# Kernel tuning notes

Hardware: AMD Instinct MI355X
Metric: run time of the kernel (lower is better)

Reference implementation:

```python
import jax, jax.numpy as jnp
from jax import lax
import numpy as np

IOU_TH = 0.5
SCORE_TH = 0.05
MAX_PER_CLASS = 10
MAX_TOTAL = 10
K_PRE = 200  # pre-NMS candidates per class (>> max_output_size_per_class)


def make_anchors(image_size: int) -> jnp.ndarray:
    """Replicates AnchorBoxes.create_anchors_boxes for square images (static shapes)."""
    aspect_ratios = [0.5, 1.0, 2.0]
    scales = [2.0 ** 0, 2.0 ** (1.0 / 3.0), 2.0 ** (2.0 / 3.0)]
    step = (image_size - 32) // 4
    areas = [(x * step + 32) ** 2 for x in range(5)]
    strides = [2 ** i for i in range(3, 8)]
    levels = []
    for l in range(5):
        fs = int(np.ceil(image_size / strides[l]))
        dims = []
        for r in aspect_ratios:  # order matches TF code: ratio outer, scale inner
            h = np.sqrt(areas[l] / r)
            w = areas[l] / h
            for s in scales:
                dims.append([s * w, s * h])
        dims = np.asarray(dims, np.float32)  # [9, 2]
        c = (np.arange(fs, dtype=np.float32) + 0.5) * strides[l]
        X, Y = np.meshgrid(c, c)  # 'xy' indexing, as in tf.meshgrid default
        centers = np.stack([X, Y], -1)  # [fs, fs, 2] (cx, cy)
        centers = np.broadcast_to(centers[:, :, None, :], (fs, fs, 9, 2))
        d = np.broadcast_to(dims[None, None], (fs, fs, 9, 2))
        levels.append(np.concatenate([centers, d], -1).reshape(-1, 4))
    return jnp.asarray(np.concatenate(levels, 0))  # [N, 4] (cx, cy, w, h)


def pairwise_iou(b):  # b: [..., K, 4] in corner format
    lt = jnp.maximum(b[..., :, None, :2], b[..., None, :, :2])
    rb = jnp.minimum(b[..., :, None, 2:], b[..., None, :, 2:])
    wh = jnp.clip(rb - lt, 0.0)
    inter = wh[..., 0] * wh[..., 1]
    area = (b[..., 2] - b[..., 0]) * (b[..., 3] - b[..., 1])
    union = area[..., :, None] + area[..., None, :] - inter
    return inter / jnp.maximum(union, 1e-8)


def setup_inputs() -> dict:
    key = jax.random.key(0)
    k1, k2 = jax.random.split(key)
    images = jax.random.normal(k1, (32, 512, 512, 3), dtype=jnp.float32)
    predictions = jax.random.normal(k2, (32, 49104, 7), dtype=jnp.float32)
    return {"images": images, "predictions": predictions}


def reference(images, predictions):
    B = predictions.shape[0]
    anchors = make_anchors(images.shape[1])  # [N, 4], static shape
    box_var = jnp.asarray([0.1, 0.1, 0.2, 0.2], predictions.dtype)

    # Decode boxes.
    bp = predictions[:, :, :4] * box_var
    cls = jax.nn.sigmoid(predictions[:, :, 4:])  # [B, N, C]
    a = anchors[None]
    xy = bp[..., :2] * a[..., 2:] + a[..., :2]
    wh = jnp.exp(bp[..., 2:]) * a[..., 2:]
    boxes = jnp.concatenate([xy - wh / 2.0, xy + wh / 2.0], -1)  # [B, N, 4] corners

    # Combined NMS (class-aware, shared boxes q=1).
    scores = jnp.transpose(cls, (0, 2, 1))  # [B, C, N]
    C = scores.shape[1]
    top_s, top_i = lax.top_k(scores, K_PRE)  # [B, C, K]
    bK = jnp.take_along_axis(boxes[:, None], top_i[..., None], axis=2)  # [B, C, K, 4]
    iou = pairwise_iou(bK)  # [B, C, K, K]
    valid = top_s >= SCORE_TH
    idx = jnp.arange(K_PRE)

    def body(i, keep):
        alive = keep[..., i][..., None]
        suppress = (iou[..., i, :] > IOU_TH) & alive & (idx > i)
        return keep & ~suppress

    keep = lax.fori_loop(0, K_PRE, body, valid)
    sel = jnp.where(keep, top_s, -1.0)

    pc_s, pc_i = lax.top_k(sel, MAX_PER_CLASS)  # [B, C, 10]
    pc_b = jnp.take_along_axis(bK, pc_i[..., None], axis=2)  # [B, C, 10, 4]
    pc_c = jnp.broadcast_to(jnp.arange(C, dtype=jnp.float32)[None, :, None], pc_s.shape)

    flat_s = pc_s.reshape(B, -1)
    flat_b = pc_b.reshape(B, -1, 4)
    flat_c = pc_c.reshape(B, -1)
    fs, fi = lax.top_k(flat_s, MAX_TOTAL)  # [B, 10]
    fb = jnp.take_along_axis(flat_b, fi[..., None], axis=1)
    fc = jnp.take_along_axis(flat_c, fi, axis=1)

    valid_mask = fs > 0.0
    nmsed_boxes = jnp.where(valid_mask[..., None], fb, 0.0)
    nmsed_scores = jnp.where(valid_mask, fs, 0.0)
    nmsed_classes = jnp.where(valid_mask, fc, 0.0)
    valid_detections = jnp.sum(valid_mask, axis=-1).astype(jnp.int32)
    return nmsed_boxes, nmsed_scores, nmsed_classes, valid_detections
```

## Files before the change

### kernel.cpp

```cpp
#include <hip/hip_runtime.h>
#include <math.h>

#define NA      49104
#define NB      32
#define KPRE    200
#define CAP     2048
#define NSLICE  64
#define NQ4     85932
#define PERQ    1344
#define STHR    448
#define TAU     2.0f
#define NBINS   512
#define SLOTCAP 64

#define WS_CNT   0
#define WS_KEYS  24576
#define WS_S10   (WS_KEYS + 96*NSLICE*SLOTCAP*8)
#define WS_B10   (WS_S10 + 96*10*4)
#define WS_DONE  (WS_B10 + 96*10*16)

__device__ __forceinline__ void anchor_of(int idx, float& cx, float& cy,
                                          float& aw, float& ah) {
    int l, r;
    if (idx < 36864)      { l = 0; r = idx; }
    else if (idx < 46080) { l = 1; r = idx - 36864; }
    else if (idx < 48384) { l = 2; r = idx - 46080; }
    else if (idx < 48960) { l = 3; r = idx - 48384; }
    else                  { l = 4; r = idx - 48960; }
    const int   fss[5]     = {64, 32, 16, 8, 4};
    const int   strides[5] = {8, 16, 32, 64, 128};
    const double areas[5]  = {1024.0, 23104.0, 73984.0, 153664.0, 262144.0};
    int a    = r % 9;
    int cell = r / 9;
    int fs   = fss[l];
    int jx   = cell % fs;
    int iy   = cell / fs;
    cx = ((float)jx + 0.5f) * (float)strides[l];
    cy = ((float)iy + 0.5f) * (float)strides[l];
    int ri = a / 3, si = a % 3;
    double ratio = (ri == 0) ? 0.5 : ((ri == 1) ? 1.0 : 2.0);
    double h = sqrt(areas[l] / ratio);
    double w = areas[l] / h;
    double s = (si == 0) ? 1.0
             : ((si == 1) ? 1.2599210498948732
                          : 1.5874010519681994);
    aw = (float)(s * w);
    ah = (float)(s * h);
}

__device__ __forceinline__ int bin_of(float x) {
    int bin = (int)floorf((x + 8.0f) * 32.0f);
    return min(max(bin, 0), NBINS - 1);
}

__device__ __forceinline__ unsigned omap(float x) {
    unsigned u = __float_as_uint(x);
    return u ^ ((u >> 31) ? 0xFFFFFFFFu : 0x80000000u);
}

__device__ __forceinline__ unsigned long long shfl_xor_u64(unsigned long long v,
                                                           int m) {
    unsigned lo = (unsigned)v, hi = (unsigned)(v >> 32);
    lo = __shfl_xor(lo, m, 64);
    hi = __shfl_xor(hi, m, 64);
    return ((unsigned long long)hi << 32) | lo;
}

__global__ __launch_bounds__(STHR) void scan_kernel(
        const float* __restrict__ pred, unsigned* __restrict__ cnts,
        unsigned long long* __restrict__ keys, unsigned* __restrict__ done) {
    const int blk = blockIdx.x;
    const int b   = blk >> 6;
    const int sl  = blk & 63;
    const int tid = threadIdx.x;

    __shared__ unsigned long long stage[3][SLOTCAP];
    __shared__ unsigned scnt[3];
    if (tid < 3) scnt[tid] = 0u;
    __syncthreads();

    const int p = tid % 7;
    int cls[4];
    #pragma unroll
    for (int j = 0; j < 4; ++j) {
        int f = (4 * p + j) % 7;
        cls[j] = (f >= 4) ? (f - 4) : -1;
    }

    const float4* row = (const float4*)(pred + (size_t)b * NA * 7);
    const int q0 = sl * PERQ + tid;
    const int q1 = q0 + STHR, q2 = q1 + STHR;
    float4 v0, v1, v2;
    bool g0 = q0 < NQ4, g1 = q1 < NQ4, g2 = q2 < NQ4;
    if (g0) v0 = row[q0];
    if (g1) v1 = row[q1];
    if (g2) v2 = row[q2];

    #pragma unroll
    for (int it = 0; it < 3; ++it) {
        bool   g = (it == 0) ? g0 : (it == 1) ? g1 : g2;
        float4 v = (it == 0) ? v0 : (it == 1) ? v1 : v2;
        int    q = (it == 0) ? q0 : (it == 1) ? q1 : q2;
        if (!g) continue;
        float vv[4] = {v.x, v.y, v.z, v.w};
        #pragma unroll
        for (int j = 0; j < 4; ++j) {
            if (cls[j] >= 0 && vv[j] >= TAU) {
                int e = (q << 2) + j;
                int n = e / 7;
                unsigned u = __float_as_uint(vv[j]) | 0x80000000u;
                unsigned long long key =
                    ((unsigned long long)(~u) << 32) | (unsigned)n;
                int c = cls[j];
                unsigned pos = atomicAdd(&scnt[c], 1u);
                if (pos < SLOTCAP) stage[c][pos] = key;
            }
        }
    }
    __syncthreads();

    if (tid < 3) cnts[(b * 3 + tid) * NSLICE + sl] = scnt[tid];
    if (tid == 3 && sl == 0) done[b] = 0u;

    #pragma unroll
    for (int c = 0; c < 3; ++c) {
        unsigned n = min(scnt[c], (unsigned)SLOTCAP);
        unsigned long long* dst =
            keys + ((size_t)(b * 3 + c) * NSLICE + sl) * SLOTCAP;
        for (unsigned i = tid; i < n; i += STHR) dst[i] = stage[c][i];
    }
}

__device__ __forceinline__ void bitonic_sort(unsigned long long* buf, unsigned P,
                                             int tid) {
    for (unsigned k = 2; k <= P; k <<= 1) {
        for (unsigned j = k >> 1; j > 0; j >>= 1) {
            for (unsigned i = tid; i < P; i += 256) {
                unsigned ixj = i ^ j;
                if (ixj > i) {
                    bool up = ((i & k) == 0);
                    unsigned long long a = buf[i], bb = buf[ixj];
                    if ((a > bb) == up) { buf[i] = bb; buf[ixj] = a; }
                }
            }
            __syncthreads();
        }
    }
}

__global__ __launch_bounds__(256) void nms_merge_kernel(
        const float* __restrict__ pred, const unsigned* __restrict__ cnts,
        const unsigned long long* __restrict__ gkeys,
        float* __restrict__ s10, float4* __restrict__ b10,
        unsigned* __restrict__ done, float* __restrict__ out) {
    const int blk = blockIdx.x;
    const int tid = threadIdx.x;

    if (blk >= 96) {
        const int b = blk - 96;
        if (tid == 0) {
            while (__hip_atomic_load(&done[b], __ATOMIC_ACQUIRE,
                                     __HIP_MEMORY_SCOPE_AGENT) < 3u)
                __builtin_amdgcn_s_sleep(8);
        }
        __syncthreads();
        __threadfence();

        if (tid < 64) {
            float s = (tid < 30) ? s10[b * 30 + tid] : -2.0f;
            float* ob = out + b * 40;
            float* os = out + 1280 + b * 10;
            float* oc = out + 1600 + b * 10;
            float* ov = out + 1920 + b;
            int valid = 0;
            for (int k = 0; k < 10; ++k) {
                unsigned u = __float_as_uint(s);
                unsigned o = (u >> 31) ? ~u : (u | 0x80000000u);
                unsigned long long key =
                    ((unsigned long long)o << 6) | (unsigned)(63 - tid);
                #pragma unroll
                for (int off = 1; off < 64; off <<= 1) {
                    unsigned long long k2 = __shfl_xor(key, off, 64);
                    key = (k2 > key) ? k2 : key;
                }
                int t = 63 - (int)(key & 63ULL);
                float best = __shfl(s, t, 64);
                bool v = best > 0.0f;
                if (tid == t) {
                    float4 bb = v ? b10[b * 30 + t] : make_float4(0, 0, 0, 0);
                    ob[k * 4 + 0] = bb.x; ob[k * 4 + 1] = bb.y;
                    ob[k * 4 + 2] = bb.z; ob[k * 4 + 3] = bb.w;
                    os[k] = v ? best : 0.0f;
                    oc[k] = v ? (float)(t / 10) : 0.0f;
                    s = -2.0f;
                }
                valid += v ? 1 : 0;
            }
            if (tid == 0) ov[0] = (float)valid;
        }
        return;
    }

    const int b = blk / 3;
    const int c = blk % 3;

    __shared__ unsigned long long keybuf[CAP];
    __shared__ unsigned long long sortbuf[512];
    __shared__ float4 boxes[KPRE];
    __shared__ float  scores_s[256];
    __shared__ unsigned long long mask[256][4];
    __shared__ unsigned hist[256];
    __shared__ unsigned hist512[NBINS];
    __shared__ unsigned Lb[NSLICE], Bb[NSLICE];
    __shared__ unsigned sMn[4], sMx[4];
    __shared__ unsigned sel_thr, sel_cnt, s_prefB, s_cumB, s_M, s_sh, s_common;
    __shared__ int sT;

    for (int i = tid; i < CAP; i += 256) keybuf[i] = ~0ULL;
    for (int i = tid; i < 512; i += 256) sortbuf[i] = ~0ULL;
    for (int i = tid; i < 256; i += 256) hist[i] = 0u;
    if (tid == 0) sel_cnt = 0u;
    __syncthreads();

    if (tid < 64) {
        unsigned L  = cnts[blk * NSLICE + tid];
        unsigned Lc = min(L, (unsigned)SLOTCAP);
        unsigned pre = Lc;
        #pragma unroll
        for (int off = 1; off < 64; off <<= 1) {
            unsigned v = __shfl_up(pre, off, 64);
            if (tid >= off) pre += v;
        }
        Lb[tid] = Lc;
        Bb[tid] = pre - Lc;
        unsigned long long ob = __ballot(L > SLOTCAP);
        if (tid == 63) s_M = pre;
        if (tid == 0)  s_common = (ob == 0ULL) ? 1u : 0u;
    }
    __syncthreads();

    const unsigned M0 = s_M;
    const bool common = s_common && M0 >= KPRE && M0 <= CAP;

    if (common) {
        const unsigned long long* src = gkeys + (size_t)blk * NSLICE * SLOTCAP;
        for (int i = tid; i < NSLICE * SLOTCAP; i += 256) {
            int sl = i >> 6, k = i & (SLOTCAP - 1);
            if ((unsigned)k < Lb[sl]) keybuf[Bb[sl] + k] = src[i];
        }
    } else {
        for (int i = tid; i < NBINS; i += 256) hist512[i] = 0u;
        if (tid == 0) s_M = 0u;
        __syncthreads();
        const float* base = pred + (size_t)b * NA * 7 + 4 + c;
        for (int n = tid; n < NA; n += 256)
            atomicAdd(&hist512[bin_of(base[(size_t)n * 7])], 1u);
        __syncthreads();
        if (tid < 64) {
            unsigned h[8]; unsigned lsum = 0;
            #pragma unroll
            for (int k = 0; k < 8; ++k) { h[k] = hist512[tid*8+k]; lsum += h[k]; }
            unsigned suf = lsum;
            #pragma unroll
            for (int off = 1; off < 64; off <<= 1) {
                unsigned v = __shfl_down(suf, off, 64);
                if (tid < 64 - off) suf += v;
            }
            unsigned acc = suf - lsum;
            #pragma unroll
            for (int k = 7; k >= 0; --k) {
                unsigned na = acc + h[k];
                if (na >= KPRE && acc < KPRE) sT = max(tid*8 + k - 1, 0);
                acc = na;
            }
        }
        __syncthreads();
        const int T = sT;
        for (int n = tid; n < NA; n += 256) {
            float x = base[(size_t)n * 7];
            if (bin_of(x) >= T) {
                unsigned long long key =
                    ((unsigned long long)(~omap(x)) << 32) | (unsigned)n;
                unsigned pos = atomicAdd(&s_M, 1u);
                if (pos < CAP) keybuf[pos] = key;
            }
        }
    }
    __syncthreads();
    const unsigned M = min(s_M, (unsigned)CAP);

    if (M > KPRE) {
        {
            unsigned mn = 0xFFu, mx = 0u;
            for (int i = tid; i < (int)M; i += 256) {
                unsigned h = (unsigned)(keybuf[i] >> 56);
                mn = min(mn, h); mx = max(mx, h);
            }
            #pragma unroll
            for (int off = 1; off < 64; off <<= 1) {
                mn = min(mn, (unsigned)__shfl_xor((int)mn, off, 64));
                mx = max(mx, (unsigned)__shfl_xor((int)mx, off, 64));
            }
            if ((tid & 63) == 0) { sMn[tid >> 6] = mn; sMx[tid >> 6] = mx; }
        }
        __syncthreads();
        if (tid == 0) {
            unsigned mn = min(min(sMn[0], sMn[1]), min(sMn[2], sMn[3]));
            unsigned mx = max(max(sMx[0], sMx[1]), max(sMx[2], sMx[3]));
            s_sh = (mn == mx) ? 40u : 48u;
        }
        __syncthreads();
        const unsigned sh = s_sh;

        for (int i = tid; i < (int)M; i += 256)
            atomicAdd(&hist[(unsigned)(keybuf[i] >> (sh + 8)) & 0xFFu], 1u);
        __syncthreads();
        if (tid < 64) {
            unsigned h0 = hist[tid*4],   h1 = hist[tid*4+1];
            unsigned h2 = hist[tid*4+2], h3 = hist[tid*4+3];
            unsigned lsum = h0 + h1 + h2 + h3;
            unsigned pre = lsum;
            #pragma unroll
            for (int off = 1; off < 64; off <<= 1) {
                unsigned v = __shfl_up(pre, off, 64);
                if (tid >= off) pre += v;
            }
            unsigned acc = pre - lsum;
            if (acc < KPRE) {
                if      (acc + h0            >= KPRE) { s_prefB = tid*4;   s_cumB = acc; }
                else if (acc + h0 + h1       >= KPRE) { s_prefB = tid*4+1; s_cumB = acc+h0; }
                else if (acc + h0 + h1 + h2  >= KPRE) { s_prefB = tid*4+2; s_cumB = acc+h0+h1; }
                else if (acc + lsum          >= KPRE) { s_prefB = tid*4+3; s_cumB = acc+h0+h1+h2; }
            }
        }
        __syncthreads();
        const unsigned B = s_prefB, before = s_cumB;
        for (int i = tid; i < 256; i += 256) hist[i] = 0u;
        __syncthreads();
        for (int i = tid; i < (int)M; i += 256) {
            unsigned long long key = keybuf[i];
            if (((unsigned)(key >> (sh + 8)) & 0xFFu) == B)
                atomicAdd(&hist[(unsigned)(key >> sh) & 0xFFu], 1u);
        }
        __syncthreads();
        if (tid < 64) {
            const unsigned target = KPRE - before;
            unsigned h0 = hist[tid*4],   h1 = hist[tid*4+1];
            unsigned h2 = hist[tid*4+2], h3 = hist[tid*4+3];
            unsigned lsum = h0 + h1 + h2 + h3;
            unsigned pre = lsum;
            #pragma unroll
            for (int off = 1; off < 64; off <<= 1) {
                unsigned v = __shfl_up(pre, off, 64);
                if (tid >= off) pre += v;
            }
            unsigned acc = pre - lsum;
            if (acc < target) {
                unsigned b2 = 256;
                if      (acc + h0           >= target) b2 = tid*4;
                else if (acc + h0 + h1      >= target) b2 = tid*4+1;
                else if (acc + h0 + h1 + h2 >= target) b2 = tid*4+2;
                else if (acc + lsum         >= target) b2 = tid*4+3;
                if (b2 < 256) sel_thr = (B << 8) | b2;
            }
        }
        __syncthreads();
        const unsigned thr = sel_thr;
        for (int i = tid; i < (int)M; i += 256) {
            unsigned long long key = keybuf[i];
            if (((unsigned)(key >> sh) & 0xFFFFu) <= thr) {
                unsigned pos = atomicAdd(&sel_cnt, 1u);
                if (pos < 512) sortbuf[pos] = key;
            }
        }
        __syncthreads();
    } else {
        for (int i = tid; i < (int)M; i += 256) sortbuf[i] = keybuf[i];
        if (tid == 0) sel_cnt = M;
        __syncthreads();
    }

    const unsigned C2 = sel_cnt;
    unsigned long long* sorted;
    if (C2 <= 256) {
        unsigned long long v = (tid < (int)C2) ? sortbuf[tid] : ~0ULL;
        __syncthreads();
        #pragma unroll
        for (unsigned k = 2; k <= 64; k <<= 1) {
            for (unsigned j = k >> 1; j > 0; j >>= 1) {
                unsigned long long o = shfl_xor_u64(v, (int)j);
                bool tm = (((tid & k) == 0) == ((tid & j) == 0));
                v = tm ? (v < o ? v : o) : (v > o ? v : o);
            }
        }
        {
            sortbuf[tid] = v; __syncthreads();
            unsigned long long o = sortbuf[tid ^ 64]; __syncthreads();
            bool tm = (((tid & 128) == 0) == ((tid & 64) == 0));
            v = tm ? (v < o ? v : o) : (v > o ? v : o);
            #pragma unroll
            for (unsigned j = 32; j > 0; j >>= 1) {
                unsigned long long o2 = shfl_xor_u64(v, (int)j);
                bool t2 = (((tid & 128) == 0) == ((tid & j) == 0));
                v = t2 ? (v < o2 ? v : o2) : (v > o2 ? v : o2);
            }
        }
        {
            sortbuf[tid] = v; __syncthreads();
            unsigned long long o = sortbuf[tid ^ 128]; __syncthreads();
            bool tm = ((tid & 128) == 0);
            v = tm ? (v < o ? v : o) : (v > o ? v : o);
            sortbuf[tid] = v; __syncthreads();
            o = sortbuf[tid ^ 64]; __syncthreads();
            tm = ((tid & 64) == 0);
            v = tm ? (v < o ? v : o) : (v > o ? v : o);
            #pragma unroll
            for (unsigned j = 32; j > 0; j >>= 1) {
                unsigned long long o2 = shfl_xor_u64(v, (int)j);
                bool t2 = ((tid & j) == 0);
                v = t2 ? (v < o2 ? v : o2) : (v > o2 ? v : o2);
            }
        }
        sortbuf[tid] = v;
        __syncthreads();
        sorted = sortbuf;
    } else if (C2 <= 512) {
        bitonic_sort(sortbuf, 512, tid);
        sorted = sortbuf;
    } else {
        bitonic_sort(keybuf, CAP, tid);
        sorted = keybuf;
    }

    if (tid < KPRE) {
        unsigned long long key = sorted[tid];
        if (key != ~0ULL) {
            unsigned n = (unsigned)key;
            unsigned v = ~(unsigned)(key >> 32);
            v = (v >> 31) ? (v ^ 0x80000000u) : ~v;
            float x  = __uint_as_float(v);
            float sc = 1.0f / (1.0f + expf(-x));
            const float* bp = pred + (size_t)b * NA * 7 + (size_t)n * 7;
            float d0 = bp[0] * 0.1f, d1 = bp[1] * 0.1f;
            float d2 = bp[2] * 0.2f, d3 = bp[3] * 0.2f;
            float cx, cy, aw, ah;
            anchor_of((int)n, cx, cy, aw, ah);
            float xx = d0 * aw + cx;
            float yy = d1 * ah + cy;
            float ww = expf(d2) * aw;
            float hh = expf(d3) * ah;
            boxes[tid]    = make_float4(xx - ww * 0.5f, yy - hh * 0.5f,
                                        xx + ww * 0.5f, yy + hh * 0.5f);
            scores_s[tid] = sc;
        } else {
            boxes[tid]    = make_float4(0, 0, 0, 0);
            scores_s[tid] = -1.0f;
        }
    } else {
        scores_s[tid] = -1.0f;
        mask[tid][0] = 0ULL; mask[tid][1] = 0ULL;
        mask[tid][2] = 0ULL; mask[tid][3] = 0ULL;
    }
    __syncthreads();

    if (tid < KPRE) {
        float4 bi = boxes[tid];
        float areai = (bi.z - bi.x) * (bi.w - bi.y);
        unsigned long long m0 = 0, m1 = 0, m2 = 0, m3 = 0;
#define IOU_CHUNK(MV, LO, HI)                                                  \
        for (int j = (tid + 1 > (LO) ? tid + 1 : (LO)); j < (HI); ++j) {       \
            float4 bj = boxes[j];                                              \
            float x1 = fmaxf(bi.x, bj.x), y1 = fmaxf(bi.y, bj.y);              \
            float x2 = fminf(bi.z, bj.z), y2 = fminf(bi.w, bj.w);              \
            float iw = fmaxf(x2 - x1, 0.0f), ih = fmaxf(y2 - y1, 0.0f);        \
            float inter = iw * ih;                                             \
            float areaj = (bj.z - bj.x) * (bj.w - bj.y);                       \
            float uni   = fmaxf(areai + areaj - inter, 1e-8f);                 \
            if (inter / uni > 0.5f) MV |= 1ULL << (j - (LO));                  \
        }
        IOU_CHUNK(m0,   0,  64)
        IOU_CHUNK(m1,  64, 128)
        IOU_CHUNK(m2, 128, 192)
        IOU_CHUNK(m3, 192, KPRE)
#undef IOU_CHUNK
        mask[tid][0] = m0; mask[tid][1] = m1;
        mask[tid][2] = m2; mask[tid][3] = m3;
    }
    __syncthreads();

    if (tid < 64) {
        const int lane = tid;
        unsigned long long keep[4];
        #pragma unroll
        for (int cb = 0; cb < 4; ++cb)
            keep[cb] = __ballot(scores_s[cb * 64 + lane] >= 0.05f);

        #pragma unroll
        for (int cb = 0; cb < 4; ++cb) {
            unsigned long long mw_self = mask[cb * 64 + lane][cb];
            unsigned long long kw   = keep[cb];
            unsigned long long work = kw & __ballot(mw_self != 0ULL);
            while (work) {
                int t = __ffsll(work) - 1;
                work &= work - 1;
                if ((kw >> t) & 1ULL) {
                    unsigned long long m = __shfl(mw_self, t, 64);
                    kw   &= ~m;
                    work &= ~m;
                }
            }
            keep[cb] = kw;
            #pragma unroll
            for (int w = cb + 1; w < 4; ++w) {
                unsigned long long myw = mask[cb * 64 + lane][w];
                if ((__ballot(myw != 0ULL) & kw) == 0ULL) continue;
                unsigned long long contrib = ((kw >> lane) & 1ULL) ? myw : 0ULL;
                #pragma unroll
                for (int off = 1; off < 64; off <<= 1)
                    contrib |= __shfl_xor(contrib, off, 64);
                keep[w] &= ~contrib;
            }
        }

        if (lane == 0) {
            int k = 0;
            #pragma unroll
            for (int cb = 0; cb < 4; ++cb) {
                unsigned long long kw = keep[cb];
                while (kw && k < 10) {
                    int t = __ffsll(kw) - 1; kw &= kw - 1;
                    int i = cb * 64 + t;
                    s10[blk * 10 + k] = scores_s[i];
                    b10[blk * 10 + k] = boxes[i];
                    ++k;
                }
            }
            #pragma unroll
            for (int cb = 0; cb < 4; ++cb) {
                unsigned long long nk = ~keep[cb];
                if (cb == 3) nk &= 0xFFULL;
                while (nk && k < 10) {
                    int t = __ffsll(nk) - 1; nk &= nk - 1;
                    int i = cb * 64 + t;
                    s10[blk * 10 + k] = -1.0f;
                    b10[blk * 10 + k] = boxes[i];
                    ++k;
                }
            }
            __threadfence();
            __hip_atomic_fetch_add(&done[b], 1u, __ATOMIC_RELEASE,
                                   __HIP_MEMORY_SCOPE_AGENT);
        }
    }
}

extern "C" void kernel_launch(void* const* d_in, const int* in_sizes, int n_in,
                              void* d_out, int out_size, void* d_ws, size_t ws_size,
                              hipStream_t stream) {
    const float* pred = (const float*)d_in[1];

    char* ws = (char*)d_ws;
    unsigned*            cnts = (unsigned*)           (ws + WS_CNT);
    unsigned long long*  keys = (unsigned long long*) (ws + WS_KEYS);
    float*               s10  = (float*)              (ws + WS_S10);
    float4*              b10  = (float4*)             (ws + WS_B10);
    unsigned*            done = (unsigned*)           (ws + WS_DONE);

    scan_kernel     <<<NB * NSLICE, STHR, 0, stream>>>(pred, cnts, keys, done);
    nms_merge_kernel<<<128, 256, 0, stream>>>(pred, cnts, keys, s10, b10, done,
                                              (float*)d_out);
}
```

Before: 65.07 us.

## Widen NMS merge blocks to 1024 threads and split IoU rows by chunk

Raises the merge kernel's block size from 256 to 1024 threads so all strided loops over keys, histograms and selection cover the data in fewer iterations. The IoU mask computation is redistributed so each thread handles one 64-column chunk of one row, which spreads the triangular work across four times as many threads. The up-front fills of the key and sort buffers are removed; padding is now written only on the bitonic paths that need it. The risks are more barriers that now synchronize 16 wavefronts, plus idle threads in the 256-wide register sort stages.

```diff
diff --git a/kernel.cpp b/kernel.cpp
--- a/kernel.cpp
+++ b/kernel.cpp
@@ -12,6 +12,7 @@
 #define TAU     2.0f
 #define NBINS   512
 #define SLOTCAP 64
+#define NTHR    1024
 
 #define WS_CNT   0
 #define WS_KEYS  24576
@@ -135,7 +136,7 @@
                                              int tid) {
     for (unsigned k = 2; k <= P; k <<= 1) {
         for (unsigned j = k >> 1; j > 0; j >>= 1) {
-            for (unsigned i = tid; i < P; i += 256) {
+            for (unsigned i = tid; i < P; i += NTHR) {
                 unsigned ixj = i ^ j;
                 if (ixj > i) {
                     bool up = ((i & k) == 0);
@@ -148,7 +149,7 @@
     }
 }
 
-__global__ __launch_bounds__(256) void nms_merge_kernel(
+__global__ __launch_bounds__(NTHR) void nms_merge_kernel(
         const float* __restrict__ pred, const unsigned* __restrict__ cnts,
         const unsigned long long* __restrict__ gkeys,
         float* __restrict__ s10, float4* __restrict__ b10,
@@ -212,15 +213,12 @@
     __shared__ unsigned hist[256];
     __shared__ unsigned hist512[NBINS];
     __shared__ unsigned Lb[NSLICE], Bb[NSLICE];
-    __shared__ unsigned sMn[4], sMx[4];
+    __shared__ unsigned sMn[16], sMx[16];
     __shared__ unsigned sel_thr, sel_cnt, s_prefB, s_cumB, s_M, s_sh, s_common;
     __shared__ int sT;
 
-    for (int i = tid; i < CAP; i += 256) keybuf[i] = ~0ULL;
-    for (int i = tid; i < 512; i += 256) sortbuf[i] = ~0ULL;
-    for (int i = tid; i < 256; i += 256) hist[i] = 0u;
+    if (tid < 256) hist[tid] = 0u;
     if (tid == 0) sel_cnt = 0u;
-    __syncthreads();
 
     if (tid < 64) {
         unsigned L  = cnts[blk * NSLICE + tid];
@@ -244,16 +242,18 @@
 
     if (common) {
         const unsigned long long* src = gkeys + (size_t)blk * NSLICE * SLOTCAP;
-        for (int i = tid; i < NSLICE * SLOTCAP; i += 256) {
+        #pragma unroll
+        for (int u = 0; u < NSLICE * SLOTCAP / NTHR; ++u) {
+            int i = u * NTHR + tid;
             int sl = i >> 6, k = i & (SLOTCAP - 1);
             if ((unsigned)k < Lb[sl]) keybuf[Bb[sl] + k] = src[i];
         }
     } else {
-        for (int i = tid; i < NBINS; i += 256) hist512[i] = 0u;
+        for (int i = tid; i < NBINS; i += NTHR) hist512[i] = 0u;
         if (tid == 0) s_M = 0u;
         __syncthreads();
         const float* base = pred + (size_t)b * NA * 7 + 4 + c;
-        for (int n = tid; n < NA; n += 256)
+        for (int n = tid; n < NA; n += NTHR)
             atomicAdd(&hist512[bin_of(base[(size_t)n * 7])], 1u);
         __syncthreads();
         if (tid < 64) {
@@ -276,7 +276,7 @@
         }
         __syncthreads();
         const int T = sT;
-        for (int n = tid; n < NA; n += 256) {
+        for (int n = tid; n < NA; n += NTHR) {
             float x = base[(size_t)n * 7];
             if (bin_of(x) >= T) {
                 unsigned long long key =
@@ -292,7 +292,7 @@
     if (M > KPRE) {
         {
             unsigned mn = 0xFFu, mx = 0u;
-            for (int i = tid; i < (int)M; i += 256) {
+            for (int i = tid; i < (int)M; i += NTHR) {
                 unsigned h = (unsigned)(keybuf[i] >> 56);
                 mn = min(mn, h); mx = max(mx, h);
             }
@@ -305,14 +305,17 @@
         }
         __syncthreads();
         if (tid == 0) {
-            unsigned mn = min(min(sMn[0], sMn[1]), min(sMn[2], sMn[3]));
-            unsigned mx = max(max(sMx[0], sMx[1]), max(sMx[2], sMx[3]));
+            unsigned mn = 0xFFu, mx = 0u;
+            #pragma unroll
+            for (int w = 0; w < NTHR / 64; ++w) {
+                mn = min(mn, sMn[w]); mx = max(mx, sMx[w]);
+            }
             s_sh = (mn == mx) ? 40u : 48u;
         }
         __syncthreads();
         const unsigned sh = s_sh;
 
-        for (int i = tid; i < (int)M; i += 256)
+        for (int i = tid; i < (int)M; i += NTHR)
             atomicAdd(&hist[(unsigned)(keybuf[i] >> (sh + 8)) & 0xFFu], 1u);
         __syncthreads();
         if (tid < 64) {
@@ -335,9 +338,9 @@
         }
         __syncthreads();
         const unsigned B = s_prefB, before = s_cumB;
-        for (int i = tid; i < 256; i += 256) hist[i] = 0u;
-        __syncthreads();
-        for (int i = tid; i < (int)M; i += 256) {
+        if (tid < 256) hist[tid] = 0u;
+        __syncthreads();
+        for (int i = tid; i < (int)M; i += NTHR) {
             unsigned long long key = keybuf[i];
             if (((unsigned)(key >> (sh + 8)) & 0xFFu) == B)
                 atomicAdd(&hist[(unsigned)(key >> sh) & 0xFFu], 1u);
@@ -366,7 +369,7 @@
         }
         __syncthreads();
         const unsigned thr = sel_thr;
-        for (int i = tid; i < (int)M; i += 256) {
+        for (int i = tid; i < (int)M; i += NTHR) {
             unsigned long long key = keybuf[i];
             if (((unsigned)(key >> sh) & 0xFFFFu) <= thr) {
                 unsigned pos = atomicAdd(&sel_cnt, 1u);
@@ -375,7 +378,7 @@
         }
         __syncthreads();
     } else {
-        for (int i = tid; i < (int)M; i += 256) sortbuf[i] = keybuf[i];
+        for (int i = tid; i < (int)M; i += NTHR) sortbuf[i] = keybuf[i];
         if (tid == 0) sel_cnt = M;
         __syncthreads();
     }
@@ -383,19 +386,23 @@
     const unsigned C2 = sel_cnt;
     unsigned long long* sorted;
     if (C2 <= 256) {
-        unsigned long long v = (tid < (int)C2) ? sortbuf[tid] : ~0ULL;
-        __syncthreads();
-        #pragma unroll
-        for (unsigned k = 2; k <= 64; k <<= 1) {
-            for (unsigned j = k >> 1; j > 0; j >>= 1) {
-                unsigned long long o = shfl_xor_u64(v, (int)j);
-                bool tm = (((tid & k) == 0) == ((tid & j) == 0));
-                v = tm ? (v < o ? v : o) : (v > o ? v : o);
-            }
-        }
-        {
-            sortbuf[tid] = v; __syncthreads();
-            unsigned long long o = sortbuf[tid ^ 64]; __syncthreads();
+        unsigned long long v = ~0ULL;
+        if (tid < 256) {
+            v = (tid < (int)C2) ? sortbuf[tid] : ~0ULL;
+            #pragma unroll
+            for (unsigned k = 2; k <= 64; k <<= 1) {
+                for (unsigned j = k >> 1; j > 0; j >>= 1) {
+                    unsigned long long o = shfl_xor_u64(v, (int)j);
+                    bool tm = (((tid & k) == 0) == ((tid & j) == 0));
+                    v = tm ? (v < o ? v : o) : (v > o ? v : o);
+                }
+            }
+        }
+        __syncthreads();
+        if (tid < 256) sortbuf[tid] = v;
+        __syncthreads();
+        if (tid < 256) {
+            unsigned long long o = sortbuf[tid ^ 64];
             bool tm = (((tid & 128) == 0) == ((tid & 64) == 0));
             v = tm ? (v < o ? v : o) : (v > o ? v : o);
             #pragma unroll
@@ -405,14 +412,20 @@
                 v = t2 ? (v < o2 ? v : o2) : (v > o2 ? v : o2);
             }
         }
-        {
-            sortbuf[tid] = v; __syncthreads();
-            unsigned long long o = sortbuf[tid ^ 128]; __syncthreads();
+        __syncthreads();
+        if (tid < 256) sortbuf[tid] = v;
+        __syncthreads();
+        if (tid < 256) {
+            unsigned long long o = sortbuf[tid ^ 128];
             bool tm = ((tid & 128) == 0);
             v = tm ? (v < o ? v : o) : (v > o ? v : o);
-            sortbuf[tid] = v; __syncthreads();
-            o = sortbuf[tid ^ 64]; __syncthreads();
-            tm = ((tid & 64) == 0);
+        }
+        __syncthreads();
+        if (tid < 256) sortbuf[tid] = v;
+        __syncthreads();
+        if (tid < 256) {
+            unsigned long long o = sortbuf[tid ^ 64];
+            bool tm = ((tid & 64) == 0);
             v = tm ? (v < o ? v : o) : (v > o ? v : o);
             #pragma unroll
             for (unsigned j = 32; j > 0; j >>= 1) {
@@ -421,13 +434,18 @@
                 v = t2 ? (v < o2 ? v : o2) : (v > o2 ? v : o2);
             }
         }
-        sortbuf[tid] = v;
+        __syncthreads();
+        if (tid < 256) sortbuf[tid] = v;
         __syncthreads();
         sorted = sortbuf;
     } else if (C2 <= 512) {
+        for (int i = (int)C2 + tid; i < 512; i += NTHR) sortbuf[i] = ~0ULL;
+        __syncthreads();
         bitonic_sort(sortbuf, 512, tid);
         sorted = sortbuf;
     } else {
+        for (int i = (int)M + tid; i < CAP; i += NTHR) keybuf[i] = ~0ULL;
+        __syncthreads();
         bitonic_sort(keybuf, CAP, tid);
         sorted = keybuf;
     }
@@ -456,35 +474,32 @@
             boxes[tid]    = make_float4(0, 0, 0, 0);
             scores_s[tid] = -1.0f;
         }
-    } else {
+    } else if (tid < 256) {
         scores_s[tid] = -1.0f;
-        mask[tid][0] = 0ULL; mask[tid][1] = 0ULL;
-        mask[tid][2] = 0ULL; mask[tid][3] = 0ULL;
     }
     __syncthreads();
 
-    if (tid < KPRE) {
-        float4 bi = boxes[tid];
-        float areai = (bi.z - bi.x) * (bi.w - bi.y);
-        unsigned long long m0 = 0, m1 = 0, m2 = 0, m3 = 0;
-#define IOU_CHUNK(MV, LO, HI)                                                  \
-        for (int j = (tid + 1 > (LO) ? tid + 1 : (LO)); j < (HI); ++j) {       \
-            float4 bj = boxes[j];                                              \
-            float x1 = fmaxf(bi.x, bj.x), y1 = fmaxf(bi.y, bj.y);              \
-            float x2 = fminf(bi.z, bj.z), y2 = fminf(bi.w, bj.w);              \
-            float iw = fmaxf(x2 - x1, 0.0f), ih = fmaxf(y2 - y1, 0.0f);        \
-            float inter = iw * ih;                                             \
-            float areaj = (bj.z - bj.x) * (bj.w - bj.y);                       \
-            float uni   = fmaxf(areai + areaj - inter, 1e-8f);                 \
-            if (inter / uni > 0.5f) MV |= 1ULL << (j - (LO));                  \
-        }
-        IOU_CHUNK(m0,   0,  64)
-        IOU_CHUNK(m1,  64, 128)
-        IOU_CHUNK(m2, 128, 192)
-        IOU_CHUNK(m3, 192, KPRE)
-#undef IOU_CHUNK
-        mask[tid][0] = m0; mask[tid][1] = m1;
-        mask[tid][2] = m2; mask[tid][3] = m3;
+    {
+        const int row = tid & 255;
+        const int cb  = tid >> 8;
+        unsigned long long m = 0ULL;
+        if (row < KPRE) {
+            const int lo = cb * 64;
+            const int hi = min(lo + 64, KPRE);
+            float4 bi = boxes[row];
+            float areai = (bi.z - bi.x) * (bi.w - bi.y);
+            for (int j = max(row + 1, lo); j < hi; ++j) {
+                float4 bj = boxes[j];
+                float x1 = fmaxf(bi.x, bj.x), y1 = fmaxf(bi.y, bj.y);
+                float x2 = fminf(bi.z, bj.z), y2 = fminf(bi.w, bj.w);
+                float iw = fmaxf(x2 - x1, 0.0f), ih = fmaxf(y2 - y1, 0.0f);
+                float inter = iw * ih;
+                float areaj = (bj.z - bj.x) * (bj.w - bj.y);
+                float uni   = fmaxf(areai + areaj - inter, 1e-8f);
+                if (inter / uni > 0.5f) m |= 1ULL << (j - lo);
+            }
+        }
+        mask[row][cb] = m;
     }
     __syncthreads();
 
@@ -567,6 +582,6 @@
     unsigned*            done = (unsigned*)           (ws + WS_DONE);
 
     scan_kernel     <<<NB * NSLICE, STHR, 0, stream>>>(pred, cnts, keys, done);
-    nms_merge_kernel<<<128, 256, 0, stream>>>(pred, cnts, keys, s10, b10, done,
-                                              (float*)d_out);
-}
+    nms_merge_kernel<<<128, NTHR, 0, stream>>>(pred, cnts, keys, s10, b10, done,
+                                               (float*)d_out);
+}
```

After: 57.04 us (median of 2 runs). 1.14x faster.
